# Optimization experiments

Hardware: AMD Instinct MI355X
Metric: run time of the kernel (lower is better)

The kernel has to match this reference:

```python
import jax, jax.numpy as jnp
import numpy as np

B, C, T = 512, 256, 256
E, K, G = 8, 5, 8
EPS = 1e-5


def setup_inputs() -> dict:
    key = jax.random.key(0)
    k1, k2, k3, k4 = jax.random.split(key, 4)
    x = jax.random.normal(k1, (B, C, T), dtype=jnp.float32)
    use_expert_i = jax.random.randint(k2, (B,), 0, E, dtype=jnp.int32)
    # per-expert Conv1d params: weight [E, Cout, Cin, K], bias [E, Cout]
    W = jax.random.normal(k3, (E, C, C, K), dtype=jnp.float32) * 0.05
    b = jax.random.normal(k4, (E, C), dtype=jnp.float32) * 0.05
    # per-expert GroupNorm affine params (torch default init: gamma=1, beta=0)
    gamma = jnp.ones((E, C), dtype=jnp.float32)
    beta = jnp.zeros((E, C), dtype=jnp.float32)
    return {"x": x, "use_expert_i": use_expert_i, "W": W, "b": b,
            "gamma": gamma, "beta": beta}


def _mish(y):
    return y * jnp.tanh(jax.nn.softplus(y))


def reference(x, use_expert_i, W, b, gamma, beta):
    # Top-1 one-hot routing => weight is exactly 1 for the selected expert, so
    # output[b] = Mish(GroupNorm(Conv1d_{e_b}(x[b]))). Gather per-sample params
    # instead of looping over experts (same math, vectorized).
    pad = K // 2
    Wb = W[use_expert_i]        # [B, Cout, Cin, K]
    bb = b[use_expert_i]        # [B, Cout]
    gb = gamma[use_expert_i]    # [B, Cout]
    betab = beta[use_expert_i]  # [B, Cout]

    def per_sample_conv(xi, wi, bi):
        # xi: [Cin, T], wi: [Cout, Cin, K] -> [Cout, T] ('same' padding)
        y = jax.lax.conv_general_dilated(xi[None], wi, window_strides=(1,),
                                         padding=[(pad, pad)])[0]
        return y + bi[:, None]

    y = jax.vmap(per_sample_conv)(x, Wb, bb)  # [B, C, T]

    # GroupNorm: normalize over (channels-in-group, length) per sample
    yg = y.reshape(B, G, C // G, T)
    mu = jnp.mean(yg, axis=(2, 3), keepdims=True)
    var = jnp.var(yg, axis=(2, 3), keepdims=True)
    yn = ((yg - mu) * jax.lax.rsqrt(var + EPS)).reshape(B, C, T)
    yn = yn * gb[:, :, None] + betab[:, :, None]
    return _mish(yn)
```

## Files before the change

### kernel.cpp

```cpp
#include <hip/hip_runtime.h>
#include <cmath>

constexpr int Bn = 512, Cn = 256, Tn = 256, En = 8;
constexpr float EPSf = 1e-5f;

using bf16x8 = __attribute__((ext_vector_type(8))) short;
using f32x4  = __attribute__((ext_vector_type(4))) float;

__device__ __forceinline__ ushort f2bf(float f) {
    uint u = __builtin_bit_cast(uint, f);
    uint r = u + 0x7FFFu + ((u >> 16) & 1u);
    return (ushort)(r >> 16);
}

__global__ __launch_bounds__(256)
void wconv_kernel(const float* __restrict__ Wf, ushort* __restrict__ Wws) {
    int idx = blockIdx.x * 256 + threadIdx.x;
    const float* src = Wf + (size_t)idx * 5;
    int ci = idx & 255, co = (idx >> 8) & 255, e = idx >> 16;
#pragma unroll
    for (int k = 0; k < 5; ++k)
        Wws[(((size_t)(e * 5 + k) * 256 + co) << 8) + ci] = f2bf(src[k]);
}

template<bool WS_W>
__global__ __launch_bounds__(256, 2)
void conv_gn_mish(const float* __restrict__ x, const int* __restrict__ expert,
                  const float* __restrict__ Wf, const ushort* __restrict__ Wws,
                  const float* __restrict__ bias, const float* __restrict__ gamma,
                  const float* __restrict__ beta, float* __restrict__ out)
{
    const int id = blockIdx.x;
    const int wg = (id & 7) * 256 + (id >> 3);
    const int b  = wg >> 2;
    const int gp = wg & 3;
    const int cb = gp * 64;
    const int e  = __builtin_amdgcn_readfirstlane(expert[b]);

    const int tid = threadIdx.x;
    const int w = tid >> 6, l = tid & 63, q = l >> 4, r = l & 15;

    __shared__ ushort xT[2][260 * 40];
    __shared__ float red[4][4];

    f32x4 acc[4][4];
#pragma unroll
    for (int m = 0; m < 4; ++m)
#pragma unroll
        for (int n = 0; n < 4; ++n) acc[m][n] = f32x4{0.f, 0.f, 0.f, 0.f};

    if (tid < 8) {
        const int bf = tid >> 2, rr = tid & 3;
        const int row = (rr < 2) ? rr : (256 + rr);
#pragma unroll
        for (int i = 0; i < 10; ++i)
            *reinterpret_cast<uint2*>(&xT[bf][row * 40 + i * 4]) = make_uint2(0u, 0u);
    }

    float v[4][8];

#define STAGE_LOAD(CI0) {                                                    \
        const float* xb = x + ((size_t)b * Cn + (CI0) + w * 8) * Tn;         \
        _Pragma("unroll")                                                    \
        for (int tt = 0; tt < 4; ++tt) {                                     \
            const int t = tt * 64 + l;                                       \
            _Pragma("unroll")                                                \
            for (int rr = 0; rr < 8; ++rr) v[tt][rr] = xb[rr * Tn + t];      \
        }                                                                    \
    }
#define STAGE_WRITE(BUF) {                                                   \
        ushort* dst = xT[BUF];                                               \
        _Pragma("unroll")                                                    \
        for (int tt = 0; tt < 4; ++tt) {                                     \
            const int t = tt * 64 + l;                                       \
            uint p0 = (uint)f2bf(v[tt][0]) | ((uint)f2bf(v[tt][1]) << 16);   \
            uint p1 = (uint)f2bf(v[tt][2]) | ((uint)f2bf(v[tt][3]) << 16);   \
            uint p2 = (uint)f2bf(v[tt][4]) | ((uint)f2bf(v[tt][5]) << 16);   \
            uint p3 = (uint)f2bf(v[tt][6]) | ((uint)f2bf(v[tt][7]) << 16);   \
            *reinterpret_cast<uint2*>(&dst[(t + 2) * 40 + w * 8])     = make_uint2(p0, p1); \
            *reinterpret_cast<uint2*>(&dst[(t + 2) * 40 + w * 8 + 4]) = make_uint2(p2, p3); \
        }                                                                    \
    }

    STAGE_LOAD(0);
    STAGE_WRITE(0);
    STAGE_LOAD(32);
    __syncthreads();

#pragma unroll 1
    for (int ct = 0; ct < 8; ++ct) {
        if (ct < 7) {
            STAGE_WRITE((ct + 1) & 1);
            if (ct < 6) STAGE_LOAD((ct + 2) * 32);
        }
        const int ci0 = ct * 32;
        const ushort* src = xT[ct & 1];

        bf16x8 A[5][4];
#pragma unroll
        for (int k = 0; k < 5; ++k) {
#pragma unroll
            for (int m = 0; m < 4; ++m) {
                if (WS_W) {
                    A[k][m] = *reinterpret_cast<const bf16x8*>(
                        Wws + (((size_t)((e * 5 + k) * 256 + cb + m * 16 + r)) << 8)
                            + ci0 + q * 8);
                } else {
                    bf16x8 a;
#pragma unroll
                    for (int j = 0; j < 8; ++j)
                        a[j] = (short)f2bf(
                            Wf[((size_t)(e * 256 + cb + m * 16 + r) * 256
                                + ci0 + q * 8 + j) * 5 + k]);
                    A[k][m] = a;
                }
            }
        }
#pragma unroll
        for (int k = 0; k < 5; ++k) {
#pragma unroll
            for (int n = 0; n < 4; ++n) {
                const bf16x8 Bf = *reinterpret_cast<const bf16x8*>(
                    &src[(w * 64 + n * 16 + r + k) * 40 + q * 8]);
#pragma unroll
                for (int m = 0; m < 4; ++m)
                    acc[m][n] = __builtin_amdgcn_mfma_f32_16x16x32_bf16(
                        A[k][m], Bf, acc[m][n], 0, 0, 0);
            }
        }
        __syncthreads();
    }
#undef STAGE_LOAD
#undef STAGE_WRITE

    float s1a = 0.f, s2a = 0.f, s1b = 0.f, s2b = 0.f;
#pragma unroll
    for (int m = 0; m < 4; ++m) {
#pragma unroll
        for (int i = 0; i < 4; ++i) {
            const float bv = bias[e * Cn + cb + m * 16 + q * 4 + i];
#pragma unroll
            for (int n = 0; n < 4; ++n) {
                const float val = acc[m][n][i] + bv;
                acc[m][n][i] = val;
                if (m < 2) { s1a += val; s2a += val * val; }
                else       { s1b += val; s2b += val * val; }
            }
        }
    }
#pragma unroll
    for (int off = 32; off; off >>= 1) {
        s1a += __shfl_xor(s1a, off); s2a += __shfl_xor(s2a, off);
        s1b += __shfl_xor(s1b, off); s2b += __shfl_xor(s2b, off);
    }
    if (l == 0) { red[w][0] = s1a; red[w][1] = s2a; red[w][2] = s1b; red[w][3] = s2b; }
    __syncthreads();
    const float S1a = red[0][0] + red[1][0] + red[2][0] + red[3][0];
    const float S2a = red[0][1] + red[1][1] + red[2][1] + red[3][1];
    const float S1b = red[0][2] + red[1][2] + red[2][2] + red[3][2];
    const float S2b = red[0][3] + red[1][3] + red[2][3] + red[3][3];

    constexpr float invn = 1.0f / (32 * 256);
    const float mua = S1a * invn, mub = S1b * invn;
    const float rsa = rsqrtf(fmaf(-mua, mua, S2a * invn) + EPSf);
    const float rsb = rsqrtf(fmaf(-mub, mub, S2b * invn) + EPSf);

#pragma unroll
    for (int m = 0; m < 4; ++m) {
        const float mu = (m < 2) ? mua : mub;
        const float rs = (m < 2) ? rsa : rsb;
#pragma unroll
        for (int i = 0; i < 4; ++i) {
            const int co = cb + m * 16 + q * 4 + i;
            const float sc = gamma[e * Cn + co] * rs;
            const float sh = beta[e * Cn + co] - mu * sc;
            float* orow = out + ((size_t)(b * Cn + co)) * Tn + w * 64 + r;
#pragma unroll
            for (int n = 0; n < 4; ++n) {
                const float y = fmaf(acc[m][n][i], sc, sh);
                const float u  = __expf(y);
                const float t2 = u * (u + 2.f);
                const float ms = (y > 20.f) ? y : y * t2 / (t2 + 2.f);
                orow[n * 16] = ms;
            }
        }
    }
}

extern "C" void kernel_launch(void* const* d_in, const int* in_sizes, int n_in,
                              void* d_out, int out_size, void* d_ws, size_t ws_size,
                              hipStream_t stream) {
    const float* x      = (const float*)d_in[0];
    const int*   expert = (const int*)  d_in[1];
    const float* Wf     = (const float*)d_in[2];
    const float* bias   = (const float*)d_in[3];
    const float* gamma  = (const float*)d_in[4];
    const float* beta   = (const float*)d_in[5];
    float* out = (float*)d_out;

    const size_t WWS_BYTES = (size_t)En * 5 * 256 * 256 * 2;

    if (ws_size >= WWS_BYTES) {
        ushort* Wws = (ushort*)d_ws;
        hipLaunchKernelGGL(wconv_kernel, dim3(2048), dim3(256), 0, stream, Wf, Wws);
        hipLaunchKernelGGL((conv_gn_mish<true>), dim3(2048), dim3(256), 0, stream,
                           x, expert, Wf, Wws, bias, gamma, beta, out);
    } else {
        hipLaunchKernelGGL((conv_gn_mish<false>), dim3(2048), dim3(256), 0, stream,
                           x, expert, Wf, nullptr, bias, gamma, beta, out);
    }
}
```

Baseline: 218.2 us.

## Pre-transpose x to bf16 [B,T,C] in a separate kernel and raise occupancy

```diff
diff --git a/kernel.cpp b/kernel.cpp
--- a/kernel.cpp
+++ b/kernel.cpp
@@ -23,9 +23,36 @@
         Wws[(((size_t)(e * 5 + k) * 256 + co) << 8) + ci] = f2bf(src[k]);
 }
 
-template<bool WS_W>
-__global__ __launch_bounds__(256, 2)
-void conv_gn_mish(const float* __restrict__ x, const int* __restrict__ expert,
+__global__ __launch_bounds__(256)
+void xpose_kernel(const float* __restrict__ x, ushort* __restrict__ xT) {
+    const int id = blockIdx.x;
+    const int b  = id >> 5;
+    const int cc = (id >> 3) & 3, tc = id & 7;
+    const int ci0 = cc * 64, t0 = tc * 32;
+    const int tid = threadIdx.x;
+
+    __shared__ float ls[64][33];
+
+    const int tl = tid & 31;
+#pragma unroll
+    for (int jj = 0; jj < 8; ++jj) {
+        const int cil = (tid >> 5) * 8 + jj;
+        ls[cil][tl] = x[((size_t)(b * 256 + ci0 + cil)) * 256 + t0 + tl];
+    }
+    __syncthreads();
+
+    const int ciw = tid & 63;
+#pragma unroll
+    for (int jj = 0; jj < 8; ++jj) {
+        const int tw = (tid >> 6) * 8 + jj;
+        xT[((size_t)(b * 256 + t0 + tw)) * 256 + ci0 + ciw] = f2bf(ls[ciw][tw]);
+    }
+}
+
+template<int MODE>
+__global__ __launch_bounds__(256, 3)
+void conv_gn_mish(const float* __restrict__ x, const ushort* __restrict__ xTw,
+                  const int* __restrict__ expert,
                   const float* __restrict__ Wf, const ushort* __restrict__ Wws,
                   const float* __restrict__ bias, const float* __restrict__ gamma,
                   const float* __restrict__ beta, float* __restrict__ out)
@@ -57,28 +84,44 @@
             *reinterpret_cast<uint2*>(&xT[bf][row * 40 + i * 4]) = make_uint2(0u, 0u);
     }
 
+    bf16x8 g[4];
     float v[4][8];
 
 #define STAGE_LOAD(CI0) {                                                    \
-        const float* xb = x + ((size_t)b * Cn + (CI0) + w * 8) * Tn;         \
-        _Pragma("unroll")                                                    \
-        for (int tt = 0; tt < 4; ++tt) {                                     \
-            const int t = tt * 64 + l;                                       \
-            _Pragma("unroll")                                                \
-            for (int rr = 0; rr < 8; ++rr) v[tt][rr] = xb[rr * Tn + t];      \
+        if (MODE == 2) {                                                     \
+            const ushort* xb = xTw + ((size_t)b * 256) * 256 + (CI0) + w * 8;\
+            _Pragma("unroll")                                                \
+            for (int tt = 0; tt < 4; ++tt)                                   \
+                g[tt] = *reinterpret_cast<const bf16x8*>(                    \
+                    xb + (size_t)(tt * 64 + l) * 256);                       \
+        } else {                                                             \
+            const float* xb = x + ((size_t)b * Cn + (CI0) + w * 8) * Tn;     \
+            _Pragma("unroll")                                                \
+            for (int tt = 0; tt < 4; ++tt) {                                 \
+                const int t = tt * 64 + l;                                   \
+                _Pragma("unroll")                                            \
+                for (int rr = 0; rr < 8; ++rr) v[tt][rr] = xb[rr * Tn + t];  \
+            }                                                                \
         }                                                                    \
     }
 #define STAGE_WRITE(BUF) {                                                   \
         ushort* dst = xT[BUF];                                               \
-        _Pragma("unroll")                                                    \
-        for (int tt = 0; tt < 4; ++tt) {                                     \
-            const int t = tt * 64 + l;                                       \
-            uint p0 = (uint)f2bf(v[tt][0]) | ((uint)f2bf(v[tt][1]) << 16);   \
-            uint p1 = (uint)f2bf(v[tt][2]) | ((uint)f2bf(v[tt][3]) << 16);   \
-            uint p2 = (uint)f2bf(v[tt][4]) | ((uint)f2bf(v[tt][5]) << 16);   \
-            uint p3 = (uint)f2bf(v[tt][6]) | ((uint)f2bf(v[tt][7]) << 16);   \
-            *reinterpret_cast<uint2*>(&dst[(t + 2) * 40 + w * 8])     = make_uint2(p0, p1); \
-            *reinterpret_cast<uint2*>(&dst[(t + 2) * 40 + w * 8 + 4]) = make_uint2(p2, p3); \
+        if (MODE == 2) {                                                     \
+            _Pragma("unroll")                                                \
+            for (int tt = 0; tt < 4; ++tt)                                   \
+                *reinterpret_cast<bf16x8*>(                                  \
+                    &dst[(tt * 64 + l + 2) * 40 + w * 8]) = g[tt];           \
+        } else {                                                             \
+            _Pragma("unroll")                                                \
+            for (int tt = 0; tt < 4; ++tt) {                                 \
+                const int t = tt * 64 + l;                                   \
+                uint p0 = (uint)f2bf(v[tt][0]) | ((uint)f2bf(v[tt][1]) << 16); \
+                uint p1 = (uint)f2bf(v[tt][2]) | ((uint)f2bf(v[tt][3]) << 16); \
+                uint p2 = (uint)f2bf(v[tt][4]) | ((uint)f2bf(v[tt][5]) << 16); \
+                uint p3 = (uint)f2bf(v[tt][6]) | ((uint)f2bf(v[tt][7]) << 16); \
+                *reinterpret_cast<uint2*>(&dst[(t + 2) * 40 + w * 8])     = make_uint2(p0, p1); \
+                *reinterpret_cast<uint2*>(&dst[(t + 2) * 40 + w * 8 + 4]) = make_uint2(p2, p3); \
+            }                                                                \
         }                                                                    \
     }
 
@@ -96,13 +139,13 @@
         const int ci0 = ct * 32;
         const ushort* src = xT[ct & 1];
 
-        bf16x8 A[5][4];
 #pragma unroll
         for (int k = 0; k < 5; ++k) {
+            bf16x8 A[4];
 #pragma unroll
             for (int m = 0; m < 4; ++m) {
-                if (WS_W) {
-                    A[k][m] = *reinterpret_cast<const bf16x8*>(
+                if (MODE >= 1) {
+                    A[m] = *reinterpret_cast<const bf16x8*>(
                         Wws + (((size_t)((e * 5 + k) * 256 + cb + m * 16 + r)) << 8)
                             + ci0 + q * 8);
                 } else {
@@ -112,12 +155,9 @@
                         a[j] = (short)f2bf(
                             Wf[((size_t)(e * 256 + cb + m * 16 + r) * 256
                                 + ci0 + q * 8 + j) * 5 + k]);
-                    A[k][m] = a;
+                    A[m] = a;
                 }
             }
-        }
-#pragma unroll
-        for (int k = 0; k < 5; ++k) {
 #pragma unroll
             for (int n = 0; n < 4; ++n) {
                 const bf16x8 Bf = *reinterpret_cast<const bf16x8*>(
@@ -125,7 +165,7 @@
 #pragma unroll
                 for (int m = 0; m < 4; ++m)
                     acc[m][n] = __builtin_amdgcn_mfma_f32_16x16x32_bf16(
-                        A[k][m], Bf, acc[m][n], 0, 0, 0);
+                        A[m], Bf, acc[m][n], 0, 0, 0);
             }
         }
         __syncthreads();
@@ -199,14 +239,22 @@
     float* out = (float*)d_out;
 
     const size_t WWS_BYTES = (size_t)En * 5 * 256 * 256 * 2;
-
-    if (ws_size >= WWS_BYTES) {
-        ushort* Wws = (ushort*)d_ws;
+    const size_t XT_BYTES  = (size_t)Bn * 256 * 256 * 2;
+
+    ushort* Wws = (ushort*)d_ws;
+    ushort* xTw = (ushort*)((char*)d_ws + WWS_BYTES);
+
+    if (ws_size >= WWS_BYTES + XT_BYTES) {
         hipLaunchKernelGGL(wconv_kernel, dim3(2048), dim3(256), 0, stream, Wf, Wws);
-        hipLaunchKernelGGL((conv_gn_mish<true>), dim3(2048), dim3(256), 0, stream,
-                           x, expert, Wf, Wws, bias, gamma, beta, out);
+        hipLaunchKernelGGL(xpose_kernel, dim3(16384), dim3(256), 0, stream, x, xTw);
+        hipLaunchKernelGGL((conv_gn_mish<2>), dim3(2048), dim3(256), 0, stream,
+                           x, xTw, expert, Wf, Wws, bias, gamma, beta, out);
+    } else if (ws_size >= WWS_BYTES) {
+        hipLaunchKernelGGL(wconv_kernel, dim3(2048), dim3(256), 0, stream, Wf, Wws);
+        hipLaunchKernelGGL((conv_gn_mish<1>), dim3(2048), dim3(256), 0, stream,
+                           x, nullptr, expert, Wf, Wws, bias, gamma, beta, out);
     } else {
-        hipLaunchKernelGGL((conv_gn_mish<false>), dim3(2048), dim3(256), 0, stream,
-                           x, expert, Wf, nullptr, bias, gamma, beta, out);
-    }
-}
+        hipLaunchKernelGGL((conv_gn_mish<0>), dim3(2048), dim3(256), 0, stream,
+                           x, nullptr, expert, Wf, nullptr, bias, gamma, beta, out);
+    }
+}
```

Result: slower. 242.9 us (+11.3%).
